# Kernel optimization log

Hardware: AMD Instinct MI355X
Metric: run time of the kernel (lower is better)

Reference implementation:

```python
import jax, jax.numpy as jnp
import numpy as np

N_EMBD = 1024
N_HEAD = 16
HEAD_DIM = N_EMBD // N_HEAD
EPS = 1e-5


def setup_inputs() -> dict:
    key = jax.random.key(0)
    ks = jax.random.split(key, 12)
    C = N_EMBD
    s = lambda fan_in: 1.0 / np.sqrt(fan_in)
    return {
        "x": jax.random.normal(ks[0], (2, 2048, C), dtype=jnp.float32),
        "ln1_g": jnp.ones((C,), jnp.float32),
        "ln1_b": jnp.zeros((C,), jnp.float32),
        "w_attn": jax.random.normal(ks[1], (C, 3 * C), jnp.float32) * s(C),
        "b_attn": jnp.zeros((3 * C,), jnp.float32),
        "w_proj": jax.random.normal(ks[2], (C, C), jnp.float32) * s(C),
        "b_proj": jnp.zeros((C,), jnp.float32),
        "ln2_g": jnp.ones((C,), jnp.float32),
        "ln2_b": jnp.zeros((C,), jnp.float32),
        "w_fc": jax.random.normal(ks[3], (C, 4 * C), jnp.float32) * s(C),
        "b_fc": jnp.zeros((4 * C,), jnp.float32),
        "w_fc2": jax.random.normal(ks[4], (4 * C, C), jnp.float32) * s(4 * C),
        "b_fc2": jnp.zeros((C,), jnp.float32),
    }


def _layernorm(x, g, b):
    mu = jnp.mean(x, axis=-1, keepdims=True)
    var = jnp.mean(jnp.square(x - mu), axis=-1, keepdims=True)
    return (x - mu) * jax.lax.rsqrt(var + EPS) * g + b


def _attention(x, w_attn, b_attn, w_proj, b_proj):
    B, T, C = x.shape
    qkv = x @ w_attn + b_attn  # [B,T,3C]
    q, k, v = jnp.split(qkv, 3, axis=-1)
    # [B,H,T,D]
    reshape = lambda t: t.reshape(B, T, N_HEAD, HEAD_DIM).transpose(0, 2, 1, 3)
    q, k, v = reshape(q), reshape(k), reshape(v)
    scale = HEAD_DIM ** (-0.5)
    att = jnp.einsum("bhqd,bhkd->bhqk", q, k) * scale  # [B,H,T,T]
    mask = jnp.tril(jnp.ones((T, T), dtype=bool))
    att = jnp.where(mask, att, -jnp.inf)
    att = jax.nn.softmax(att, axis=-1)
    y = jnp.einsum("bhqk,bhkd->bhqd", att, v)
    y = y.transpose(0, 2, 1, 3).reshape(B, T, C)
    return y @ w_proj + b_proj


def _mlp(x, w_fc, b_fc, w_fc2, b_fc2):
    h = jax.nn.gelu(x @ w_fc + b_fc, approximate=False)  # nn.GELU default = exact erf
    return h @ w_fc2 + b_fc2


def reference(x, ln1_g, ln1_b, w_attn, b_attn, w_proj, b_proj,
              ln2_g, ln2_b, w_fc, b_fc, w_fc2, b_fc2):
    x = x + _attention(_layernorm(x, ln1_g, ln1_b), w_attn, b_attn, w_proj, b_proj)
    x = x + _mlp(_layernorm(x, ln2_g, ln2_b), w_fc, b_fc, w_fc2, b_fc2)
    return x
```

## Files before the change

kernel.cpp:

```cpp
#include <hip/hip_runtime.h>
#include <hip/hip_bf16.h>
#include <math.h>

typedef __attribute__((ext_vector_type(8))) __bf16 bf16x8;
typedef __attribute__((ext_vector_type(4))) float floatx4;
typedef __attribute__((ext_vector_type(8))) unsigned short ushort8;

#define C_EMBD 1024
#define T_SEQ 2048
#define NH 16
#define HD 64

static __device__ __forceinline__ unsigned short f2b(float f) {
  __hip_bfloat16 h = __float2bfloat16(f);
  unsigned short u;
  __builtin_memcpy(&u, &h, sizeof(u));
  return u;
}
static __device__ __forceinline__ float b2f(unsigned short u) {
  unsigned int b = ((unsigned int)u) << 16;
  float f;
  __builtin_memcpy(&f, &b, sizeof(f));
  return f;
}

static __device__ __forceinline__ void gload16(const void* g, void* l) {
  __builtin_amdgcn_global_load_lds(
      (__attribute__((address_space(1))) void*)(void*)g,
      (__attribute__((address_space(3))) void*)l, 16, 0, 0);
}

static __device__ __forceinline__ floatx4 mfma_bf16(bf16x8 a, bf16x8 b, floatx4 c) {
  return __builtin_amdgcn_mfma_f32_16x16x32_bf16(a, b, c, 0, 0, 0);
}

__global__ __launch_bounds__(256) void wtrans(const float* __restrict__ in,
                                              unsigned short* __restrict__ out,
                                              int K, int N) {
  __shared__ float t[32][33];
  int n0 = blockIdx.x * 32, k0 = blockIdx.y * 32;
  int tx = threadIdx.x & 31, ty = threadIdx.x >> 5;
#pragma unroll
  for (int i = 0; i < 4; i++)
    t[ty + i * 8][tx] = in[(size_t)(k0 + ty + i * 8) * N + n0 + tx];
  __syncthreads();
#pragma unroll
  for (int i = 0; i < 4; i++)
    out[(size_t)(n0 + ty + i * 8) * K + k0 + tx] = f2b(t[tx][ty + i * 8]);
}

__global__ __launch_bounds__(256) void ln_fwd(const float* __restrict__ x,
                                              const float* __restrict__ g,
                                              const float* __restrict__ bta,
                                              unsigned short* __restrict__ out) {
  int row = blockIdx.x;
  int t = threadIdx.x;
  const float4* xr = (const float4*)(x + (size_t)row * C_EMBD);
  float4 v = xr[t];
  float s = v.x + v.y + v.z + v.w;
  float ss = v.x * v.x + v.y * v.y + v.z * v.z + v.w * v.w;
#pragma unroll
  for (int m = 1; m < 64; m <<= 1) {
    s += __shfl_xor(s, m, 64);
    ss += __shfl_xor(ss, m, 64);
  }
  __shared__ float ps[8];
  int wv = t >> 6;
  if ((t & 63) == 0) { ps[wv] = s; ps[4 + wv] = ss; }
  __syncthreads();
  s = ps[0] + ps[1] + ps[2] + ps[3];
  ss = ps[4] + ps[5] + ps[6] + ps[7];
  float mu = s * (1.0f / C_EMBD);
  float var = ss * (1.0f / C_EMBD) - mu * mu;
  float rs = rsqrtf(var + 1e-5f);
  float4 gv = ((const float4*)g)[t];
  float4 bv = ((const float4*)bta)[t];
  ushort4 o;
  o.x = f2b((v.x - mu) * rs * gv.x + bv.x);
  o.y = f2b((v.y - mu) * rs * gv.y + bv.y);
  o.z = f2b((v.z - mu) * rs * gv.z + bv.z);
  o.w = f2b((v.w - mu) * rs * gv.w + bv.w);
  *(ushort4*)(out + (size_t)row * C_EMBD + t * 4) = o;
}

template <int EP, int MI>
__global__ __launch_bounds__(256) void gemm_bt(const unsigned short* __restrict__ A,
                                               const unsigned short* __restrict__ Bt,
                                               const float* __restrict__ bias,
                                               const float* __restrict__ res,
                                               void* __restrict__ outv,
                                               unsigned short* __restrict__ vt,
                                               int M, int N, int K) {
  __shared__ __align__(16) unsigned short As[MI * 32 * 32];
  __shared__ __align__(16) unsigned short Bs[128 * 32];
  const int tid = threadIdx.x;
  const int wv = tid >> 6, ln = tid & 63;
  const int quad = ln >> 4, l15 = ln & 15;
  const int wm = wv >> 1, wn = wv & 1;
  const int m0 = blockIdx.y * (MI * 32), n0 = blockIdx.x * 128;

  floatx4 acc[MI][4];
#pragma unroll
  for (int i = 0; i < MI; i++)
#pragma unroll
    for (int j = 0; j < 4; j++) acc[i][j] = (floatx4)0.0f;

  const int rowA = ln >> 2;
  const int koff = (ln & 3) * 8;

  for (int k0 = 0; k0 < K; k0 += 32) {
    if (k0) __syncthreads();
#pragma unroll
    for (int hh = 0; hh < MI / 2; ++hh) {
      int r = hh * 64 + wv * 16 + rowA;
      gload16(A + (size_t)(m0 + r) * K + k0 + koff, &As[(hh * 64 + wv * 16) * 32]);
    }
#pragma unroll
    for (int hh = 0; hh < 2; ++hh) {
      int r = hh * 64 + wv * 16 + rowA;
      gload16(Bt + (size_t)(n0 + r) * K + k0 + koff, &Bs[(hh * 64 + wv * 16) * 32]);
    }
    __syncthreads();
    bf16x8 af[MI], bfr[4];
#pragma unroll
    for (int mi = 0; mi < MI; mi++)
      af[mi] = *(const bf16x8*)&As[(wm * (MI * 16) + mi * 16 + l15) * 32 + quad * 8];
#pragma unroll
    for (int ni = 0; ni < 4; ni++)
      bfr[ni] = *(const bf16x8*)&Bs[(wn * 64 + ni * 16 + l15) * 32 + quad * 8];
#pragma unroll
    for (int mi = 0; mi < MI; mi++)
#pragma unroll
      for (int ni = 0; ni < 4; ni++)
        acc[mi][ni] = mfma_bf16(af[mi], bfr[ni], acc[mi][ni]);
  }

#pragma unroll
  for (int mi = 0; mi < MI; mi++) {
#pragma unroll
    for (int ni = 0; ni < 4; ni++) {
      int col = n0 + wn * 64 + ni * 16 + l15;
      int rowb = m0 + wm * (MI * 16) + mi * 16 + quad * 4;
      float bc = bias[col];
      if (EP == 1) {
#pragma unroll
        for (int r = 0; r < 4; r++) {
          size_t idx = (size_t)(rowb + r) * N + col;
          ((float*)outv)[idx] = acc[mi][ni][r] + bc + res[idx];
        }
      } else if (EP == 2) {
#pragma unroll
        for (int r = 0; r < 4; r++) {
          float v = acc[mi][ni][r] + bc;
          v = 0.5f * v * (1.0f + erff(v * 0.70710678118f));
          ((unsigned short*)outv)[(size_t)(rowb + r) * N + col] = f2b(v);
        }
      } else {
        if (col < 2048) {
#pragma unroll
          for (int r = 0; r < 4; r++)
            ((unsigned short*)outv)[(size_t)(rowb + r) * N + col] =
                f2b(acc[mi][ni][r] + bc);
        } else {
          int dall = col - 2048;
          int hh2 = dall >> 6, dd = dall & 63;
          int bq = rowb >> 11, t0 = rowb & 2047;
          __align__(8) unsigned short pk[4];
#pragma unroll
          for (int r = 0; r < 4; r++) pk[r] = f2b(acc[mi][ni][r] + bc);
          *(ushort4*)&vt[(size_t)((bq * NH + hh2) * HD + dd) * T_SEQ + t0] =
              *(const ushort4*)pk;
        }
      }
    }
  }
}

__global__ __launch_bounds__(256) void attn_fwd(const unsigned short* __restrict__ qkv,
                                                const unsigned short* __restrict__ vt,
                                                unsigned short* __restrict__ y) {
  __shared__ __align__(16) unsigned short Ks[64 * 64];
  __shared__ __align__(16) unsigned short Vs[64 * 64];
  __shared__ __align__(16) unsigned short Ps[4 * 16 * 72];
  const int tid = threadIdx.x;
  const int wv = tid >> 6, ln = tid & 63;
  const int quad = ln >> 4, l15 = ln & 15;
  const int pair = blockIdx.x, h = blockIdx.y, b = blockIdx.z;
  unsigned short* Pw = &Ps[wv * 16 * 72];

  const unsigned short* kbase = qkv + (size_t)b * T_SEQ * 3072 + 1024 + h * HD;
  const unsigned short* vbase = vt + (size_t)(b * NH + h) * HD * T_SEQ;

  int koffs[2], voffs[2], ldst[2];
#pragma unroll
  for (int g = 0; g < 2; g++) {
    int S = wv * 128 + g * 64 + ln;
    int r = S >> 3;
    int c = (S & 7) ^ (r & 7);
    koffs[g] = r * 3072 + c * 8;
    voffs[g] = r * T_SEQ + c * 8;
    ldst[g] = wv * 1024 + g * 512;
  }

  for (int ph = 0; ph < 2; ++ph) {
    const int qt = ph ? (31 - pair) : pair;
    const unsigned short* qp =
        qkv + (size_t)(b * T_SEQ + qt * 64 + wv * 16 + l15) * 3072 + h * HD;
    bf16x8 qf[2];
#pragma unroll
    for (int kc = 0; kc < 2; kc++) {
      ushort8 u = *(const ushort8*)(qp + kc * 32 + quad * 8);
      union { ushort8 u; bf16x8 v; } cv;
#pragma unroll
      for (int j = 0; j < 8; j++) cv.u[j] = f2b(b2f(u[j]) * 0.18033688f);
      qf[kc] = cv.v;
    }

    floatx4 o[4];
#pragma unroll
    for (int dt = 0; dt < 4; dt++) o[dt] = (floatx4)0.0f;
    float lacc = 0.0f;

    auto step = [&](int kt, bool diag) {
      __syncthreads();
#pragma unroll
      for (int g = 0; g < 2; g++) {
        gload16(kbase + (size_t)(kt * 64) * 3072 + koffs[g], &Ks[ldst[g]]);
        gload16(vbase + kt * 64 + voffs[g], &Vs[ldst[g]]);
      }
      __syncthreads();

      floatx4 s[4];
#pragma unroll
      for (int nt = 0; nt < 4; nt++) s[nt] = (floatx4)0.0f;
#pragma unroll
      for (int nt = 0; nt < 4; nt++)
#pragma unroll
        for (int kc = 0; kc < 2; kc++) {
          bf16x8 kf = *(const bf16x8*)
              &Ks[(nt * 16 + l15) * 64 + (((kc * 4 + quad) ^ (l15 & 7)) * 8)];
          s[nt] = mfma_bf16(kf, qf[kc], s[nt]);
        }

      float psum = 0.0f;
#pragma unroll
      for (int nt = 0; nt < 4; nt++) {
        __align__(8) unsigned short pk[4];
#pragma unroll
        for (int r = 0; r < 4; r++) {
          float sv = s[nt][r];
          if (diag && (nt * 16 + quad * 4 + r > wv * 16 + l15)) sv = -1e30f;
          float p = exp2f(sv - 12.0f);
          psum += p;
          pk[r] = f2b(p);
        }
        *(ushort4*)&Pw[l15 * 72 + nt * 16 + quad * 4] = *(const ushort4*)pk;
      }
      lacc += psum;

      bf16x8 pf0 = *(const bf16x8*)&Pw[l15 * 72 + quad * 8];
      bf16x8 pf1 = *(const bf16x8*)&Pw[l15 * 72 + 32 + quad * 8];
#pragma unroll
      for (int dt = 0; dt < 4; dt++) {
        bf16x8 vf0 = *(const bf16x8*)
            &Vs[(dt * 16 + l15) * 64 + ((quad ^ (l15 & 7)) * 8)];
        bf16x8 vf1 = *(const bf16x8*)
            &Vs[(dt * 16 + l15) * 64 + (((4 + quad) ^ (l15 & 7)) * 8)];
        o[dt] = mfma_bf16(vf0, pf0, o[dt]);
        o[dt] = mfma_bf16(vf1, pf1, o[dt]);
      }
    };

    for (int kt = 0; kt < qt; ++kt) step(kt, false);
    step(qt, true);

    lacc += __shfl_xor(lacc, 16, 64);
    lacc += __shfl_xor(lacc, 32, 64);
    float rinv = 1.0f / lacc;
#pragma unroll
    for (int dt = 0; dt < 4; dt++) {
      __align__(8) unsigned short ov[4];
#pragma unroll
      for (int r = 0; r < 4; r++) ov[r] = f2b(o[dt][r] * rinv);
      *(ushort4*)&y[(size_t)(b * T_SEQ + qt * 64 + wv * 16 + l15) * C_EMBD +
                    h * HD + dt * 16 + quad * 4] = *(const ushort4*)ov;
    }
  }
}

extern "C" void kernel_launch(void* const* d_in, const int* in_sizes, int n_in,
                              void* d_out, int out_size, void* d_ws, size_t ws_size,
                              hipStream_t stream) {
  (void)in_sizes; (void)n_in; (void)out_size; (void)ws_size;
  const float* x      = (const float*)d_in[0];
  const float* ln1_g  = (const float*)d_in[1];
  const float* ln1_b  = (const float*)d_in[2];
  const float* w_attn = (const float*)d_in[3];
  const float* b_attn = (const float*)d_in[4];
  const float* w_proj = (const float*)d_in[5];
  const float* b_proj = (const float*)d_in[6];
  const float* ln2_g  = (const float*)d_in[7];
  const float* ln2_b  = (const float*)d_in[8];
  const float* w_fc   = (const float*)d_in[9];
  const float* b_fc   = (const float*)d_in[10];
  const float* w_fc2  = (const float*)d_in[11];
  const float* b_fc2  = (const float*)d_in[12];
  float* out = (float*)d_out;

  char* ws = (char*)d_ws;
  unsigned short* wat  = (unsigned short*)ws; ws += (size_t)3072 * 1024 * 2;
  unsigned short* wpt  = (unsigned short*)ws; ws += (size_t)1024 * 1024 * 2;
  unsigned short* wft  = (unsigned short*)ws; ws += (size_t)4096 * 1024 * 2;
  unsigned short* wf2t = (unsigned short*)ws; ws += (size_t)1024 * 4096 * 2;
  unsigned short* xn   = (unsigned short*)ws; ws += (size_t)4096 * 1024 * 2;
  unsigned short* qkv  = (unsigned short*)ws; ws += (size_t)4096 * 3072 * 2;
  unsigned short* yat  = (unsigned short*)ws; ws += (size_t)4096 * 1024 * 2;
  unsigned short* hbuf = (unsigned short*)ws; ws += (size_t)4096 * 4096 * 2;
  unsigned short* vt = hbuf;

  wtrans<<<dim3(3072 / 32, 1024 / 32), 256, 0, stream>>>(w_attn, wat, 1024, 3072);
  wtrans<<<dim3(1024 / 32, 1024 / 32), 256, 0, stream>>>(w_proj, wpt, 1024, 1024);
  wtrans<<<dim3(4096 / 32, 1024 / 32), 256, 0, stream>>>(w_fc, wft, 1024, 4096);
  wtrans<<<dim3(1024 / 32, 4096 / 32), 256, 0, stream>>>(w_fc2, wf2t, 4096, 1024);

  ln_fwd<<<4096, 256, 0, stream>>>(x, ln1_g, ln1_b, xn);
  gemm_bt<3, 4><<<dim3(24, 32), 256, 0, stream>>>(
      xn, wat, b_attn, nullptr, qkv, vt, 4096, 3072, 1024);
  attn_fwd<<<dim3(16, NH, 2), 256, 0, stream>>>(qkv, vt, yat);
  gemm_bt<1, 2><<<dim3(8, 64), 256, 0, stream>>>(
      yat, wpt, b_proj, x, out, nullptr, 4096, 1024, 1024);
  ln_fwd<<<4096, 256, 0, stream>>>(out, ln2_g, ln2_b, xn);
  gemm_bt<2, 4><<<dim3(32, 32), 256, 0, stream>>>(
      xn, wft, b_fc, nullptr, hbuf, nullptr, 4096, 4096, 1024);
  gemm_bt<1, 2><<<dim3(8, 64), 256, 0, stream>>>(
      hbuf, wf2t, b_fc2, out, out, nullptr, 4096, 1024, 4096);
}
```

Baseline: 386.1 us.

## Add 256x256-tile double-buffered GEMM with swizzled LDS for QKV and FC

Adds a new 512-thread GEMM kernel using 256x256 output tiles, a 64-wide K step, double-buffered LDS staging via direct global-to-LDS loads, XOR-swizzled LDS layout, XCD-aware block remapping, and raised wave priority around the MFMA bursts. It replaces the older gemm_bt for the QKV projection and the first MLP matmul. The aim is more data reuse per tile and overlap of loads with compute. The trade-off is large register and LDS use, and few workgroups (192/256) relative to the CU count, which can hurt occupancy and tail balance.

```diff
diff --git a/kernel.cpp b/kernel.cpp
--- a/kernel.cpp
+++ b/kernel.cpp
@@ -142,6 +142,144 @@
       int col = n0 + wn * 64 + ni * 16 + l15;
       int rowb = m0 + wm * (MI * 16) + mi * 16 + quad * 4;
       float bc = bias[col];
+      if (EP == 1) {
+#pragma unroll
+        for (int r = 0; r < 4; r++) {
+          size_t idx = (size_t)(rowb + r) * N + col;
+          ((float*)outv)[idx] = acc[mi][ni][r] + bc + res[idx];
+        }
+      } else if (EP == 2) {
+#pragma unroll
+        for (int r = 0; r < 4; r++) {
+          float v = acc[mi][ni][r] + bc;
+          v = 0.5f * v * (1.0f + erff(v * 0.70710678118f));
+          ((unsigned short*)outv)[(size_t)(rowb + r) * N + col] = f2b(v);
+        }
+      } else {
+        if (col < 2048) {
+#pragma unroll
+          for (int r = 0; r < 4; r++)
+            ((unsigned short*)outv)[(size_t)(rowb + r) * N + col] =
+                f2b(acc[mi][ni][r] + bc);
+        } else {
+          int dall = col - 2048;
+          int hh2 = dall >> 6, dd = dall & 63;
+          int bq = rowb >> 11, t0 = rowb & 2047;
+          __align__(8) unsigned short pk[4];
+#pragma unroll
+          for (int r = 0; r < 4; r++) pk[r] = f2b(acc[mi][ni][r] + bc);
+          *(ushort4*)&vt[(size_t)((bq * NH + hh2) * HD + dd) * T_SEQ + t0] =
+              *(const ushort4*)pk;
+        }
+      }
+    }
+  }
+}
+
+template <int EP>
+__global__ __launch_bounds__(512, 2) void gemm256(
+    const unsigned short* __restrict__ A, const unsigned short* __restrict__ Bt,
+    const float* __restrict__ bias, const float* __restrict__ res,
+    void* __restrict__ outv, unsigned short* __restrict__ vt,
+    int M, int N, int K) {
+  __shared__ __align__(16) unsigned short As[2][256 * 64];
+  __shared__ __align__(16) unsigned short Bs[2][256 * 64];
+  const int tid = threadIdx.x;
+  const int wv = tid >> 6, ln = tid & 63;
+  const int quad = ln >> 4, l15 = ln & 15;
+  const int wm = wv >> 2, wn = wv & 3;
+
+  const int gx = gridDim.x;
+  const int nwg = gx * gridDim.y;
+  int id = blockIdx.y * gx + blockIdx.x;
+  const int cpx = nwg >> 3;
+  id = (id & 7) * cpx + (id >> 3);
+  const int n0 = (id % gx) * 256;
+  const int m0 = (id / gx) * 256;
+
+  const int srow = wv * 8 + (ln >> 3);
+  const int skch = ((ln & 7) ^ (ln >> 3)) * 8;
+  const unsigned short* aSt = A + (size_t)(m0 + srow) * K + skch;
+  const unsigned short* bSt = Bt + (size_t)(n0 + srow) * K + skch;
+  const size_t gstr = (size_t)64 * K;
+
+  const int xsw = (l15 & 7) * 8;
+  const int csw0 = (quad * 8) ^ xsw;
+  const int csw1 = (32 + quad * 8) ^ xsw;
+
+  floatx4 acc[8][4];
+#pragma unroll
+  for (int i = 0; i < 8; i++)
+#pragma unroll
+    for (int j = 0; j < 4; j++) acc[i][j] = (floatx4)0.0f;
+
+  const int NT = K >> 6;
+
+  auto stage = [&](int bi, int kt) {
+    const unsigned short* aS = aSt + kt * 64;
+    const unsigned short* bS = bSt + kt * 64;
+    unsigned short* Ad = &As[bi][wv * 512];
+    unsigned short* Bd = &Bs[bi][wv * 512];
+#pragma unroll
+    for (int g = 0; g < 4; g++) {
+      gload16(aS + (size_t)g * gstr, Ad + g * 4096);
+      gload16(bS + (size_t)g * gstr, Bd + g * 4096);
+    }
+  };
+
+  stage(0, 0);
+  asm volatile("s_waitcnt vmcnt(0)" ::: "memory");
+  __builtin_amdgcn_s_barrier();
+
+  for (int t = 0; t < NT; ++t) {
+    const int cur = t & 1;
+    const unsigned short* Ac = As[cur];
+    const unsigned short* Bc = Bs[cur];
+    bf16x8 bF[4][2];
+#pragma unroll
+    for (int q = 0; q < 4; q++) {
+      bf16x8 aF[2][2];
+      if (q == 0) {
+        if (t + 1 < NT) stage(cur ^ 1, t + 1);
+#pragma unroll
+        for (int ni = 0; ni < 4; ni++) {
+          const unsigned short* r = Bc + (wn * 64 + ni * 16 + l15) * 64;
+          bF[ni][0] = *(const bf16x8*)(r + csw0);
+          bF[ni][1] = *(const bf16x8*)(r + csw1);
+        }
+      }
+#pragma unroll
+      for (int m2 = 0; m2 < 2; m2++) {
+        const unsigned short* r = Ac + (wm * 128 + (q * 2 + m2) * 16 + l15) * 64;
+        aF[m2][0] = *(const bf16x8*)(r + csw0);
+        aF[m2][1] = *(const bf16x8*)(r + csw1);
+      }
+      __builtin_amdgcn_s_barrier();
+      asm volatile("s_waitcnt lgkmcnt(0)" ::: "memory");
+      __builtin_amdgcn_sched_barrier(0);
+      __builtin_amdgcn_s_setprio(1);
+#pragma unroll
+      for (int kk = 0; kk < 2; kk++)
+#pragma unroll
+        for (int m2 = 0; m2 < 2; m2++)
+#pragma unroll
+          for (int ni = 0; ni < 4; ni++)
+            acc[q * 2 + m2][ni] =
+                mfma_bf16(aF[m2][kk], bF[ni][kk], acc[q * 2 + m2][ni]);
+      __builtin_amdgcn_s_setprio(0);
+      __builtin_amdgcn_s_barrier();
+    }
+    asm volatile("s_waitcnt vmcnt(0)" ::: "memory");
+    __builtin_amdgcn_s_barrier();
+  }
+
+#pragma unroll
+  for (int mi = 0; mi < 8; mi++) {
+#pragma unroll
+    for (int ni = 0; ni < 4; ni++) {
+      const int col = n0 + wn * 64 + ni * 16 + l15;
+      const int rowb = m0 + wm * 128 + mi * 16 + quad * 4;
+      const float bc = bias[col];
       if (EP == 1) {
 #pragma unroll
         for (int r = 0; r < 4; r++) {
@@ -324,13 +462,13 @@
   wtrans<<<dim3(1024 / 32, 4096 / 32), 256, 0, stream>>>(w_fc2, wf2t, 4096, 1024);
 
   ln_fwd<<<4096, 256, 0, stream>>>(x, ln1_g, ln1_b, xn);
-  gemm_bt<3, 4><<<dim3(24, 32), 256, 0, stream>>>(
+  gemm256<3><<<dim3(3072 / 256, 4096 / 256), 512, 0, stream>>>(
       xn, wat, b_attn, nullptr, qkv, vt, 4096, 3072, 1024);
   attn_fwd<<<dim3(16, NH, 2), 256, 0, stream>>>(qkv, vt, yat);
   gemm_bt<1, 2><<<dim3(8, 64), 256, 0, stream>>>(
       yat, wpt, b_proj, x, out, nullptr, 4096, 1024, 1024);
   ln_fwd<<<4096, 256, 0, stream>>>(out, ln2_g, ln2_b, xn);
-  gemm_bt<2, 4><<<dim3(32, 32), 256, 0, stream>>>(
+  gemm256<2><<<dim3(4096 / 256, 4096 / 256), 512, 0, stream>>>(
       xn, wft, b_fc, nullptr, hbuf, nullptr, 4096, 4096, 1024);
   gemm_bt<1, 2><<<dim3(8, 64), 256, 0, stream>>>(
       hbuf, wf2t, b_fc2, out, out, nullptr, 4096, 1024, 4096);
```

Result: no change. 393.5 us (+1.9%).
